# Kernel optimization log

Measured on AMD Instinct MI355X. Metric: run time of the kernel, lower is better.

The kernel has to match this reference:

```python
import jax, jax.numpy as jnp
import numpy as np

B, T, L, INPUT_DIM = 16, 128, 100, 100
EMB = 100
FEAT = INPUT_DIM + 3 * EMB          # 400
HID, OUT = 128, 50
RNN_IN = 2 * INPUT_DIM + 3 * L      # 500
VOCAB = 10000 + 2


def setup_inputs() -> dict:
    key = jax.random.key(0)
    ks = jax.random.split(key, 12)
    first = jax.random.normal(ks[0], (B, T, INPUT_DIM), jnp.float32)
    idx = jax.random.randint(ks[1], (B, T, 3 * L), 0, VOCAB).astype(jnp.float32)
    x = jnp.concatenate([first, idx], axis=2)  # [B,T,400]
    s = 0.05
    return {
        "x": x,
        "embed_nodes": jax.random.normal(ks[2], (VOCAB, EMB), jnp.float32) * s,
        "embed_paths": jax.random.normal(ks[3], (VOCAB, EMB), jnp.float32) * s,
        "W_t": jax.random.normal(ks[4], (FEAT, FEAT), jnp.float32) / np.sqrt(FEAT),
        "b_t": jnp.zeros((FEAT,), jnp.float32),
        "W_a": jax.random.normal(ks[5], (FEAT, 1), jnp.float32) / np.sqrt(FEAT),
        "b_a": jnp.zeros((1,), jnp.float32),
        "W_ih": jax.random.normal(ks[6], (4 * HID, RNN_IN), jnp.float32) / np.sqrt(RNN_IN),
        "W_hh": jax.random.normal(ks[7], (4 * HID, HID), jnp.float32) / np.sqrt(HID),
        "b_ih": jnp.zeros((4 * HID,), jnp.float32),
        "b_hh": jnp.zeros((4 * HID,), jnp.float32),
        "W_fc": jax.random.normal(ks[8], (HID, OUT), jnp.float32) / np.sqrt(HID),
        "b_fc": jnp.zeros((OUT,), jnp.float32),
    }


def _lstm(xs, W_ih, W_hh, b_ih, b_hh):
    # xs: [B,T,D] -> out [B,T,H]; PyTorch gate order i,f,g,o
    def step(carry, xt):
        h, c = carry
        g = xt @ W_ih.T + h @ W_hh.T + (b_ih + b_hh)  # [B,4H]
        i, f, gg, o = jnp.split(g, 4, axis=-1)
        c = jax.nn.sigmoid(f) * c + jax.nn.sigmoid(i) * jnp.tanh(gg)
        h = jax.nn.sigmoid(o) * jnp.tanh(c)
        return (h, c), h
    h0 = jnp.zeros((xs.shape[0], HID), xs.dtype)
    (_, _), hs = jax.lax.scan(step, (h0, h0), jnp.swapaxes(xs, 0, 1))
    return jnp.swapaxes(hs, 0, 1)


def reference(x, embed_nodes, embed_paths, W_t, b_t, W_a, b_a,
              W_ih, W_hh, b_ih, b_hh, W_fc, b_fc):
    first = x[:, :, :INPUT_DIM]                                   # [B,T,100]
    c2v = x[:, :, INPUT_DIM:INPUT_DIM + 3 * L].reshape(B, T, L, 3).astype(jnp.int32)
    s_emb = embed_nodes[c2v[..., 0]]                              # [B,T,L,100]
    e_emb = embed_nodes[c2v[..., 2]]
    p_emb = embed_paths[c2v[..., 1]]
    att_part = jnp.broadcast_to(first[:, :, None, :], (B, T, L, INPUT_DIM))
    full = jnp.concatenate([s_emb, e_emb, p_emb, att_part], axis=3)  # [B,T,L,400]
    # dropout skipped (deterministic reference == evaluating=True path)
    transformed = jnp.tanh(full @ W_t + b_t)
    ctx = transformed @ W_a + b_a                                 # [B,T,L,1]
    # faithful to nn.Softmax(dim=1): softmax over the sequence axis T
    attn = jax.nn.softmax(ctx, axis=1)
    code_vectors = jnp.sum(full * attn, axis=2)                   # [B,T,400]
    rnn_input = jnp.concatenate([first, code_vectors], axis=2)    # [B,T,500]
    out = _lstm(rnn_input, W_ih, W_hh, b_ih, b_hh)                # [B,T,128]
    return jax.nn.sigmoid(out @ W_fc + b_fc)                      # [B,T,50]
```

## Files before the change

### kernel.cpp

```cpp
#include <hip/hip_runtime.h>
#include <hip/hip_bf16.h>
#include <stdint.h>

#define B_     16
#define T_     128
#define L_     100
#define IN_    100
#define EMB_   100
#define FEAT_  400
#define HID_   128
#define OUT_   50
#define RNNIN_ 500
#define VOCAB_ 10002
#define BT_    2048
#define TBLK   157

#define S_T    (0.16f / 127.0f)
#define INVS_T (127.0f / 0.16f)
#define S_E    (0.30f / 127.0f)
#define INVS_E (127.0f / 0.30f)

typedef __attribute__((ext_vector_type(8))) short short8;
typedef __attribute__((ext_vector_type(4))) float f32x4;

__device__ __forceinline__ float fast_tanh(float x) {
    x = fminf(15.f, fmaxf(-15.f, x));
    float e = __expf(2.f * x);
    return (e - 1.f) * __builtin_amdgcn_rcpf(e + 1.f);
}
__device__ __forceinline__ float sigm(float x) {
    x = fminf(30.f, fmaxf(-30.f, x));
    float e = __expf(-x);
    return __builtin_amdgcn_rcpf(1.f + e);
}
__device__ __forceinline__ signed char q8(float v, float invs) {
    float t = fminf(127.f, fmaxf(-127.f, v * invs));
    return (signed char)__float2int_rn(t);
}
__device__ __forceinline__ int sb(unsigned int u, int k) {
    return (int)(signed char)(u >> (8 * k));
}

__global__ __launch_bounds__(256) void casts_k(
    const float* __restrict__ EN, const float* __restrict__ EP,
    const float* __restrict__ Wt, const float* __restrict__ Wih,
    const float* __restrict__ Whh,
    signed char* __restrict__ EN8, signed char* __restrict__ EP8,
    __hip_bfloat16* __restrict__ WtT, __hip_bfloat16* __restrict__ Wih_bf,
    __hip_bfloat16* __restrict__ Whh_bf)
{
    int t0 = blockIdx.x * 256 + threadIdx.x;
    const int stride = 1024 * 256;
    int n1 = VOCAB_ * 100;
    for (int i = t0; i < n1; i += stride) EN8[i] = q8(EN[i], INVS_E);
    for (int i = t0; i < n1; i += stride) EP8[i] = q8(EP[i], INVS_E);
    for (int i = t0; i < 4 * 400 * 128; i += stride) {
        int w = i / (400 * 128), rem = i - w * 400 * 128;
        int n = rem >> 7, k = rem & 127;
        WtT[i] = __float2bfloat16((k < 100) ? Wt[(size_t)(w * 100 + k) * 400 + n] : 0.f);
    }
    for (int i = t0; i < 512 * 512; i += stride) {
        int g = i >> 9, k = i & 511;
        Wih_bf[i] = __float2bfloat16((k < 500) ? Wih[(size_t)g * 500 + k] : 0.f);
    }
    for (int i = t0; i < 512 * 128; i += stride) Whh_bf[i] = __float2bfloat16(Whh[i]);
}

__device__ __forceinline__ void load_a100_f32(const float* __restrict__ arow,
                                              int kg, short8 af[4])
{
#pragma unroll
    for (int s = 0; s < 3; s++) {
        const float* p = arow + s * 32 + kg * 8;
#pragma unroll
        for (int j = 0; j < 8; j++)
            af[s][j] = (short)__bfloat16_as_ushort(__float2bfloat16(p[j]));
    }
    short8 z = {};
    af[3] = z;
    if (kg == 0) {
#pragma unroll
        for (int j = 0; j < 4; j++)
            af[3][j] = (short)__bfloat16_as_ushort(__float2bfloat16(arow[96 + j]));
    }
}

__global__ __launch_bounds__(256) void mm_k(
    const float* __restrict__ EN, const float* __restrict__ EP,
    const float* __restrict__ x, const __hip_bfloat16* __restrict__ WtT,
    const float* __restrict__ btb,
    signed char* __restrict__ Es, signed char* __restrict__ Ee,
    signed char* __restrict__ Ep, float* __restrict__ q)
{
    int blk = blockIdx.x, tid = threadIdx.x;
    int wave = tid >> 6, lane = tid & 63;
    int cl = lane & 15, kg = lane >> 4;

    if (blk < 3 * TBLK) {
        int which = blk / TBLK, mb = blk - which * TBLK;
        const float* A = (which == 2) ? EP : EN;
        signed char* outp = (which == 0) ? Es : ((which == 1) ? Ee : Ep);
        int r0 = mb * 64 + wave * 16;
        int ra = r0 + cl; if (ra > VOCAB_ - 1) ra = VOCAB_ - 1;
        short8 af[4];
        load_a100_f32(A + (size_t)ra * 100, kg, af);
        const __hip_bfloat16* Bp = WtT + (size_t)which * 400 * 128;
        for (int n0 = 0; n0 < 25; n0++) {
            const __hip_bfloat16* brow = Bp + (size_t)(n0 * 16 + cl) * 128 + kg * 8;
            f32x4 acc = (f32x4){0.f, 0.f, 0.f, 0.f};
            acc = __builtin_amdgcn_mfma_f32_16x16x32_bf16(af[0], *(const short8*)(brow), acc, 0, 0, 0);
            acc = __builtin_amdgcn_mfma_f32_16x16x32_bf16(af[1], *(const short8*)(brow + 32), acc, 0, 0, 0);
            acc = __builtin_amdgcn_mfma_f32_16x16x32_bf16(af[2], *(const short8*)(brow + 64), acc, 0, 0, 0);
            acc = __builtin_amdgcn_mfma_f32_16x16x32_bf16(af[3], *(const short8*)(brow + 96), acc, 0, 0, 0);
            int colj = n0 * 16 + cl;
#pragma unroll
            for (int r = 0; r < 4; r++) {
                int gr = r0 + kg * 4 + r;
                if (gr < VOCAB_)
                    outp[(size_t)gr * 400 + colj] = q8(acc[r], INVS_T);
            }
        }
    } else {
        int mb = blk - 3 * TBLK;
        int r0 = mb * 64 + wave * 16;
        short8 af[4];
        load_a100_f32(x + (size_t)(r0 + cl) * 400, kg, af);
        const __hip_bfloat16* Bp = WtT + (size_t)3 * 400 * 128;
        for (int n0 = 0; n0 < 25; n0++) {
            const __hip_bfloat16* brow = Bp + (size_t)(n0 * 16 + cl) * 128 + kg * 8;
            f32x4 acc = (f32x4){0.f, 0.f, 0.f, 0.f};
            acc = __builtin_amdgcn_mfma_f32_16x16x32_bf16(af[0], *(const short8*)(brow), acc, 0, 0, 0);
            acc = __builtin_amdgcn_mfma_f32_16x16x32_bf16(af[1], *(const short8*)(brow + 32), acc, 0, 0, 0);
            acc = __builtin_amdgcn_mfma_f32_16x16x32_bf16(af[2], *(const short8*)(brow + 64), acc, 0, 0, 0);
            acc = __builtin_amdgcn_mfma_f32_16x16x32_bf16(af[3], *(const short8*)(brow + 96), acc, 0, 0, 0);
            int colj = n0 * 16 + cl;
            float bb = btb[colj];
#pragma unroll
            for (int r = 0; r < 4; r++) {
                int gr = r0 + kg * 4 + r;
                q[(size_t)gr * 400 + colj] = acc[r] + bb;
            }
        }
    }
}

__global__ __launch_bounds__(256) void stage_a(
    const float* __restrict__ x,
    const signed char* __restrict__ Es8, const signed char* __restrict__ Ee8,
    const signed char* __restrict__ Ep8,
    const float* __restrict__ q, const float* __restrict__ Wa,
    float* __restrict__ ctx)
{
    __shared__ int idx_s[300];
    int bt = blockIdx.x, tid = threadIdx.x;
    const float* xr = x + (size_t)bt * 400 + 100;
    for (int i = tid; i < 300; i += 256) idx_s[i] = (int)xr[i];
    int lane = tid & 63, wave = tid >> 6;
    bool act = lane < 50;
    int j0 = lane * 8;
    float qv[8], wv[8];
    if (act) {
        float4 qa = *(const float4*)(q + (size_t)bt * 400 + j0);
        float4 qb = *(const float4*)(q + (size_t)bt * 400 + j0 + 4);
        float4 wa = *(const float4*)(Wa + j0);
        float4 wb = *(const float4*)(Wa + j0 + 4);
        qv[0]=qa.x; qv[1]=qa.y; qv[2]=qa.z; qv[3]=qa.w;
        qv[4]=qb.x; qv[5]=qb.y; qv[6]=qb.z; qv[7]=qb.w;
        wv[0]=wa.x; wv[1]=wa.y; wv[2]=wa.z; wv[3]=wa.w;
        wv[4]=wb.x; wv[5]=wb.y; wv[6]=wb.z; wv[7]=wb.w;
    } else {
#pragma unroll
        for (int jj = 0; jj < 8; jj++) { qv[jj] = 0.f; wv[jj] = 0.f; }
    }
    __syncthreads();
    for (int l = wave; l < 100; l += 4) {
        int i0 = idx_s[3 * l], i1 = idx_s[3 * l + 1], i2 = idx_s[3 * l + 2];
        float sum = 0.f;
        if (act) {
            uint2 a  = ((const uint2*)(Es8 + (size_t)i0 * 400))[lane];
            uint2 b  = ((const uint2*)(Ee8 + (size_t)i2 * 400))[lane];
            uint2 cc = ((const uint2*)(Ep8 + (size_t)i1 * 400))[lane];
            int zi[8];
#pragma unroll
            for (int k = 0; k < 4; k++) {
                zi[k]     = sb(a.x, k) + sb(b.x, k) + sb(cc.x, k);
                zi[4 + k] = sb(a.y, k) + sb(b.y, k) + sb(cc.y, k);
            }
#pragma unroll
            for (int jj = 0; jj < 8; jj++) {
                float z = fmaf((float)zi[jj], S_T, qv[jj]);
                sum = fmaf(fast_tanh(z), wv[jj], sum);
            }
        }
#pragma unroll
        for (int off = 32; off; off >>= 1) sum += __shfl_xor(sum, off);
        if (lane == 0) ctx[(size_t)bt * 100 + l] = sum;
    }
}

__global__ __launch_bounds__(256) void softmax_w(
    const float* __restrict__ ctx, float* __restrict__ attn)
{
    int wid = blockIdx.x * 4 + (threadIdx.x >> 6);
    int lane = threadIdx.x & 63;
    int b = wid / 100, l = wid - b * 100;
    size_t base = (size_t)b * 128 * 100 + l;
    float v0 = ctx[base + (size_t)lane * 100];
    float v1 = ctx[base + (size_t)(lane + 64) * 100];
    float m = fmaxf(v0, v1);
#pragma unroll
    for (int off = 32; off; off >>= 1) m = fmaxf(m, __shfl_xor(m, off));
    float e0 = __expf(v0 - m), e1 = __expf(v1 - m);
    float s = e0 + e1;
#pragma unroll
    for (int off = 32; off; off >>= 1) s += __shfl_xor(s, off);
    float rs = 1.f / s;
    attn[base + (size_t)lane * 100] = e0 * rs;
    attn[base + (size_t)(lane + 64) * 100] = e1 * rs;
}

__global__ __launch_bounds__(128) void stage_c(
    const float* __restrict__ x, const float* __restrict__ attn,
    const signed char* __restrict__ EN8, const signed char* __restrict__ EP8,
    __hip_bfloat16* __restrict__ rnn_bf)
{
    __shared__ float at[100];
    __shared__ int idx[300];
    int bt = blockIdx.x, tid = threadIdx.x;
    if (tid < 100) at[tid] = attn[(size_t)bt * 100 + tid];
    const float* xr = x + (size_t)bt * 400 + 100;
    for (int i = tid; i < 300; i += 128) idx[i] = (int)xr[i];
    __syncthreads();
    int d = tid;
    __hip_bfloat16* o = rnn_bf + (size_t)bt * 512;
    if (d < 100) {
        float as = 0.f, ae = 0.f, ap = 0.f, sa = 0.f;
#pragma unroll 4
        for (int l = 0; l < 100; l++) {
            float a = at[l]; sa += a;
            as = fmaf(a, (float)EN8[(size_t)idx[3 * l] * 100 + d], as);
            ae = fmaf(a, (float)EN8[(size_t)idx[3 * l + 2] * 100 + d], ae);
            ap = fmaf(a, (float)EP8[(size_t)idx[3 * l + 1] * 100 + d], ap);
        }
        float fi = x[(size_t)bt * 400 + d];
        o[d]       = __float2bfloat16(fi);
        o[100 + d] = __float2bfloat16(as * S_E);
        o[200 + d] = __float2bfloat16(ae * S_E);
        o[300 + d] = __float2bfloat16(ap * S_E);
        o[400 + d] = __float2bfloat16(fi * sa);
    } else if (d < 112) {
        o[400 + d] = __float2bfloat16(0.f);
    }
}

__global__ __launch_bounds__(512, 1) void lstm_k(
    const __hip_bfloat16* __restrict__ rnn_bf, const __hip_bfloat16* __restrict__ Wih_bf,
    const float* __restrict__ bih, const float* __restrict__ bhh,
    const __hip_bfloat16* __restrict__ Whh_bf,
    float* __restrict__ X, float* __restrict__ hs)
{
    int b = blockIdx.x, tid = threadIdx.x;
    int wave = tid >> 6, lane = tid & 63;
    int col = lane & 15, kg = lane >> 4;

    {
        int r0 = b * 128 + wave * 16;
        short8 af[16];
        const __hip_bfloat16* arow = rnn_bf + (size_t)(r0 + col) * 512 + kg * 8;
#pragma unroll
        for (int ks = 0; ks < 16; ks++) af[ks] = *(const short8*)(arow + ks * 32);
        for (int n0 = 0; n0 < 32; n0 += 2) {
            const __hip_bfloat16* b0 = Wih_bf + (size_t)(n0 * 16 + col) * 512 + kg * 8;
            const __hip_bfloat16* b1 = b0 + 16 * 512;
            f32x4 acA = (f32x4){0.f, 0.f, 0.f, 0.f};
            f32x4 acB = (f32x4){0.f, 0.f, 0.f, 0.f};
#pragma unroll
            for (int ks = 0; ks < 16; ks++) {
                acA = __builtin_amdgcn_mfma_f32_16x16x32_bf16(af[ks], *(const short8*)(b0 + ks * 32), acA, 0, 0, 0);
                acB = __builtin_amdgcn_mfma_f32_16x16x32_bf16(af[ks], *(const short8*)(b1 + ks * 32), acB, 0, 0, 0);
            }
            int c0 = n0 * 16 + col, c1 = c0 + 16;
            float bi0 = bih[c0] + bhh[c0];
            float bi1 = bih[c1] + bhh[c1];
#pragma unroll
            for (int r = 0; r < 4; r++) {
                int m = r0 + kg * 4 + r;
                X[(size_t)m * 512 + c0] = acA[r] + bi0;
                X[(size_t)m * 512 + c1] = acB[r] + bi1;
            }
        }
    }

    short8 bf[4][4];
#pragma unroll
    for (int n = 0; n < 4; n++) {
        int g = n * 128 + wave * 16 + col;
#pragma unroll
        for (int kk = 0; kk < 4; kk++)
            bf[n][kk] = *(const short8*)(Whh_bf + (size_t)g * 128 + kk * 32 + kg * 8);
    }

    __shared__ __hip_bfloat16 hbuf[2][128];
    __shared__ float Xs[16][512];
    __shared__ float hsb_s[16][128];
    float c = 0.f;
    if (tid < 128) hbuf[0][tid] = __float2bfloat16(0.f);
    const float* xb = X + (size_t)b * 128 * 512;
    float* hb = hs + (size_t)b * 128 * 128;
    int j = wave * 16 + col;
    int p = 0;

    __syncthreads();

    for (int tc = 0; tc < 8; tc++) {
        {
            const float* src = xb + (size_t)tc * 16 * 512 + tid;
#pragma unroll
            for (int k = 0; k < 16; k++) Xs[k][tid] = src[k * 512];
        }
        __syncthreads();

#pragma unroll 1
        for (int ts = 0; ts < 16; ts++) {
            short8 af[4];
            short8 zz = {};
#pragma unroll
            for (int kk = 0; kk < 4; kk++) {
                af[kk] = zz;
                if (col == 0) af[kk] = *(const short8*)(&hbuf[p][0] + kk * 32 + kg * 8);
            }
            f32x4 acc[4];
#pragma unroll
            for (int n = 0; n < 4; n++) acc[n] = (f32x4){0.f, 0.f, 0.f, 0.f};
#pragma unroll
            for (int kk = 0; kk < 4; kk++)
#pragma unroll
                for (int n = 0; n < 4; n++)
                    acc[n] = __builtin_amdgcn_mfma_f32_16x16x32_bf16(af[kk], bf[n][kk], acc[n], 0, 0, 0);

            if (lane < 16) {
                float pi = acc[0][0] + Xs[ts][j];
                float pf = acc[1][0] + Xs[ts][128 + j];
                float pg = acc[2][0] + Xs[ts][256 + j];
                float po = acc[3][0] + Xs[ts][384 + j];
                c = sigm(pf) * c + sigm(pi) * fast_tanh(pg);
                float hn = sigm(po) * fast_tanh(c);
                hbuf[p ^ 1][j] = __float2bfloat16(hn);
                hsb_s[ts][j] = hn;
            }
            __syncthreads();
            p ^= 1;
        }

        {
            float* dst = hb + (size_t)tc * 16 * 128;
#pragma unroll
            for (int k = 0; k < 4; k++) {
                int i = k * 512 + tid;
                dst[i] = hsb_s[i >> 7][i & 127];
            }
        }
    }
}

__global__ __launch_bounds__(64) void fc_k(
    const float* __restrict__ hs, const float* __restrict__ Wfc,
    const float* __restrict__ bfc, float* __restrict__ out)
{
    int r0 = blockIdx.x * 4, o = threadIdx.x;
    if (o >= 50) return;
    float acc[4] = {0.f, 0.f, 0.f, 0.f};
    for (int j = 0; j < 128; j++) {
        float wv = Wfc[j * 50 + o];
#pragma unroll
        for (int r = 0; r < 4; r++)
            acc[r] = fmaf(hs[(size_t)(r0 + r) * 128 + j], wv, acc[r]);
    }
    float bb = bfc[o];
#pragma unroll
    for (int r = 0; r < 4; r++) out[(size_t)(r0 + r) * 50 + o] = sigm(acc[r] + bb);
}

extern "C" void kernel_launch(void* const* d_in, const int* in_sizes, int n_in,
                              void* d_out, int out_size, void* d_ws, size_t ws_size,
                              hipStream_t stream) {
    const float* x   = (const float*)d_in[0];
    const float* EN  = (const float*)d_in[1];
    const float* EP  = (const float*)d_in[2];
    const float* Wt  = (const float*)d_in[3];
    const float* bt  = (const float*)d_in[4];
    const float* Wa  = (const float*)d_in[5];
    const float* Wih = (const float*)d_in[7];
    const float* Whh = (const float*)d_in[8];
    const float* bih = (const float*)d_in[9];
    const float* bhh = (const float*)d_in[10];
    const float* Wfc = (const float*)d_in[11];
    const float* bfc = (const float*)d_in[12];
    float* out = (float*)d_out;

    char* ws = (char*)d_ws;
    size_t off = 0;
    auto alloc = [&](size_t bytes) -> char* {
        char* p = ws + off;
        off = (off + bytes + 255) & ~(size_t)255;
        return p;
    };
    signed char* Es  = (signed char*)alloc((size_t)VOCAB_ * 400);
    signed char* Ee  = (signed char*)alloc((size_t)VOCAB_ * 400);
    signed char* Epb = (signed char*)alloc((size_t)VOCAB_ * 400);
    signed char* EN8 = (signed char*)alloc((size_t)VOCAB_ * 100);
    signed char* EP8 = (signed char*)alloc((size_t)VOCAB_ * 100);
    __hip_bfloat16* WtT    = (__hip_bfloat16*)alloc((size_t)4 * 400 * 128 * 2);
    __hip_bfloat16* Wih_bf = (__hip_bfloat16*)alloc((size_t)512 * 512 * 2);
    __hip_bfloat16* Whh_bf = (__hip_bfloat16*)alloc((size_t)512 * 128 * 2);
    __hip_bfloat16* rnn_bf = (__hip_bfloat16*)alloc((size_t)BT_ * 512 * 2);
    float* q    = (float*)alloc((size_t)BT_ * 400 * 4);
    float* ctx  = (float*)alloc((size_t)BT_ * 100 * 4);
    float* attn = (float*)alloc((size_t)BT_ * 100 * 4);
    float* X    = (float*)alloc((size_t)BT_ * 512 * 4);
    float* hsb  = (float*)alloc((size_t)BT_ * 128 * 4);

    casts_k<<<1024, 256, 0, stream>>>(EN, EP, Wt, Wih, Whh,
                                      EN8, EP8, WtT, Wih_bf, Whh_bf);
    mm_k<<<3 * TBLK + 32, 256, 0, stream>>>(EN, EP, x, WtT, bt,
                                            Es, Ee, Epb, q);
    stage_a<<<BT_, 256, 0, stream>>>(x, Es, Ee, Epb, q, Wa, ctx);
    softmax_w<<<400, 256, 0, stream>>>(ctx, attn);
    stage_c<<<BT_, 128, 0, stream>>>(x, attn, EN8, EP8, rnn_bf);
    lstm_k<<<B_, 512, 0, stream>>>(rnn_bf, Wih_bf, bih, bhh, Whh_bf, X, hsb);
    fc_k<<<BT_ / 4, 64, 0, stream>>>(hsb, Wfc, bfc, out);
}
```

Before: 314.3 us.

## Split LSTM input projection into separate GEMM kernel and drop int8 embedding casts

Moves the input-to-gate GEMM out of the 16-block LSTM kernel into its own 32-block kernel, so the projection runs across more compute units instead of only the 16 recurrence blocks. It also removes the int8 quantization pass over both embedding tables; stage_c now gathers fp32 embeddings directly, and the casts kernel shrinks to 256 blocks. The trade-off is an extra launch and fp32 gather traffic four times larger in stage_c, in exchange for skipping a full-table conversion every call and gaining precision.

```diff
diff --git a/kernel.cpp b/kernel.cpp
--- a/kernel.cpp
+++ b/kernel.cpp
@@ -17,8 +17,6 @@
 
 #define S_T    (0.16f / 127.0f)
 #define INVS_T (127.0f / 0.16f)
-#define S_E    (0.30f / 127.0f)
-#define INVS_E (127.0f / 0.30f)
 
 typedef __attribute__((ext_vector_type(8))) short short8;
 typedef __attribute__((ext_vector_type(4))) float f32x4;
@@ -42,18 +40,13 @@
 }
 
 __global__ __launch_bounds__(256) void casts_k(
-    const float* __restrict__ EN, const float* __restrict__ EP,
     const float* __restrict__ Wt, const float* __restrict__ Wih,
     const float* __restrict__ Whh,
-    signed char* __restrict__ EN8, signed char* __restrict__ EP8,
     __hip_bfloat16* __restrict__ WtT, __hip_bfloat16* __restrict__ Wih_bf,
     __hip_bfloat16* __restrict__ Whh_bf)
 {
     int t0 = blockIdx.x * 256 + threadIdx.x;
-    const int stride = 1024 * 256;
-    int n1 = VOCAB_ * 100;
-    for (int i = t0; i < n1; i += stride) EN8[i] = q8(EN[i], INVS_E);
-    for (int i = t0; i < n1; i += stride) EP8[i] = q8(EP[i], INVS_E);
+    const int stride = 256 * 256;
     for (int i = t0; i < 4 * 400 * 128; i += stride) {
         int w = i / (400 * 128), rem = i - w * 400 * 128;
         int n = rem >> 7, k = rem & 127;
@@ -221,7 +214,7 @@
 
 __global__ __launch_bounds__(128) void stage_c(
     const float* __restrict__ x, const float* __restrict__ attn,
-    const signed char* __restrict__ EN8, const signed char* __restrict__ EP8,
+    const float* __restrict__ EN, const float* __restrict__ EP,
     __hip_bfloat16* __restrict__ rnn_bf)
 {
     __shared__ float at[100];
@@ -238,58 +231,65 @@
 #pragma unroll 4
         for (int l = 0; l < 100; l++) {
             float a = at[l]; sa += a;
-            as = fmaf(a, (float)EN8[(size_t)idx[3 * l] * 100 + d], as);
-            ae = fmaf(a, (float)EN8[(size_t)idx[3 * l + 2] * 100 + d], ae);
-            ap = fmaf(a, (float)EP8[(size_t)idx[3 * l + 1] * 100 + d], ap);
+            as = fmaf(a, EN[(size_t)idx[3 * l] * 100 + d], as);
+            ae = fmaf(a, EN[(size_t)idx[3 * l + 2] * 100 + d], ae);
+            ap = fmaf(a, EP[(size_t)idx[3 * l + 1] * 100 + d], ap);
         }
         float fi = x[(size_t)bt * 400 + d];
         o[d]       = __float2bfloat16(fi);
-        o[100 + d] = __float2bfloat16(as * S_E);
-        o[200 + d] = __float2bfloat16(ae * S_E);
-        o[300 + d] = __float2bfloat16(ap * S_E);
+        o[100 + d] = __float2bfloat16(as);
+        o[200 + d] = __float2bfloat16(ae);
+        o[300 + d] = __float2bfloat16(ap);
         o[400 + d] = __float2bfloat16(fi * sa);
     } else if (d < 112) {
         o[400 + d] = __float2bfloat16(0.f);
     }
 }
 
-__global__ __launch_bounds__(512, 1) void lstm_k(
+__global__ __launch_bounds__(256) void gemm_x(
     const __hip_bfloat16* __restrict__ rnn_bf, const __hip_bfloat16* __restrict__ Wih_bf,
     const float* __restrict__ bih, const float* __restrict__ bhh,
-    const __hip_bfloat16* __restrict__ Whh_bf,
-    float* __restrict__ X, float* __restrict__ hs)
+    float* __restrict__ X)
+{
+    int blk = blockIdx.x, tid = threadIdx.x;
+    int wave = tid >> 6, lane = tid & 63;
+    int cl = lane & 15, kg = lane >> 4;
+    int r0 = blk * 64 + wave * 16;
+
+    short8 af[16];
+    const __hip_bfloat16* arow = rnn_bf + (size_t)(r0 + cl) * 512 + kg * 8;
+#pragma unroll
+    for (int ks = 0; ks < 16; ks++) af[ks] = *(const short8*)(arow + ks * 32);
+
+    for (int n0 = 0; n0 < 32; n0 += 2) {
+        const __hip_bfloat16* b0 = Wih_bf + (size_t)(n0 * 16 + cl) * 512 + kg * 8;
+        const __hip_bfloat16* b1 = b0 + 16 * 512;
+        f32x4 acA = (f32x4){0.f, 0.f, 0.f, 0.f};
+        f32x4 acB = (f32x4){0.f, 0.f, 0.f, 0.f};
+#pragma unroll
+        for (int ks = 0; ks < 16; ks++) {
+            acA = __builtin_amdgcn_mfma_f32_16x16x32_bf16(af[ks], *(const short8*)(b0 + ks * 32), acA, 0, 0, 0);
+            acB = __builtin_amdgcn_mfma_f32_16x16x32_bf16(af[ks], *(const short8*)(b1 + ks * 32), acB, 0, 0, 0);
+        }
+        int c0 = n0 * 16 + cl, c1 = c0 + 16;
+        float bi0 = bih[c0] + bhh[c0];
+        float bi1 = bih[c1] + bhh[c1];
+#pragma unroll
+        for (int r = 0; r < 4; r++) {
+            int m = r0 + kg * 4 + r;
+            X[(size_t)m * 512 + c0] = acA[r] + bi0;
+            X[(size_t)m * 512 + c1] = acB[r] + bi1;
+        }
+    }
+}
+
+__global__ __launch_bounds__(512, 1) void lstm_k(
+    const float* __restrict__ X, const __hip_bfloat16* __restrict__ Whh_bf,
+    float* __restrict__ hs)
 {
     int b = blockIdx.x, tid = threadIdx.x;
     int wave = tid >> 6, lane = tid & 63;
     int col = lane & 15, kg = lane >> 4;
-
-    {
-        int r0 = b * 128 + wave * 16;
-        short8 af[16];
-        const __hip_bfloat16* arow = rnn_bf + (size_t)(r0 + col) * 512 + kg * 8;
-#pragma unroll
-        for (int ks = 0; ks < 16; ks++) af[ks] = *(const short8*)(arow + ks * 32);
-        for (int n0 = 0; n0 < 32; n0 += 2) {
-            const __hip_bfloat16* b0 = Wih_bf + (size_t)(n0 * 16 + col) * 512 + kg * 8;
-            const __hip_bfloat16* b1 = b0 + 16 * 512;
-            f32x4 acA = (f32x4){0.f, 0.f, 0.f, 0.f};
-            f32x4 acB = (f32x4){0.f, 0.f, 0.f, 0.f};
-#pragma unroll
-            for (int ks = 0; ks < 16; ks++) {
-                acA = __builtin_amdgcn_mfma_f32_16x16x32_bf16(af[ks], *(const short8*)(b0 + ks * 32), acA, 0, 0, 0);
-                acB = __builtin_amdgcn_mfma_f32_16x16x32_bf16(af[ks], *(const short8*)(b1 + ks * 32), acB, 0, 0, 0);
-            }
-            int c0 = n0 * 16 + col, c1 = c0 + 16;
-            float bi0 = bih[c0] + bhh[c0];
-            float bi1 = bih[c1] + bhh[c1];
-#pragma unroll
-            for (int r = 0; r < 4; r++) {
-                int m = r0 + kg * 4 + r;
-                X[(size_t)m * 512 + c0] = acA[r] + bi0;
-                X[(size_t)m * 512 + c1] = acB[r] + bi1;
-            }
-        }
-    }
 
     short8 bf[4][4];
 #pragma unroll
@@ -408,8 +408,6 @@
     signed char* Es  = (signed char*)alloc((size_t)VOCAB_ * 400);
     signed char* Ee  = (signed char*)alloc((size_t)VOCAB_ * 400);
     signed char* Epb = (signed char*)alloc((size_t)VOCAB_ * 400);
-    signed char* EN8 = (signed char*)alloc((size_t)VOCAB_ * 100);
-    signed char* EP8 = (signed char*)alloc((size_t)VOCAB_ * 100);
     __hip_bfloat16* WtT    = (__hip_bfloat16*)alloc((size_t)4 * 400 * 128 * 2);
     __hip_bfloat16* Wih_bf = (__hip_bfloat16*)alloc((size_t)512 * 512 * 2);
     __hip_bfloat16* Whh_bf = (__hip_bfloat16*)alloc((size_t)512 * 128 * 2);
@@ -420,13 +418,13 @@
     float* X    = (float*)alloc((size_t)BT_ * 512 * 4);
     float* hsb  = (float*)alloc((size_t)BT_ * 128 * 4);
 
-    casts_k<<<1024, 256, 0, stream>>>(EN, EP, Wt, Wih, Whh,
-                                      EN8, EP8, WtT, Wih_bf, Whh_bf);
+    casts_k<<<256, 256, 0, stream>>>(Wt, Wih, Whh, WtT, Wih_bf, Whh_bf);
     mm_k<<<3 * TBLK + 32, 256, 0, stream>>>(EN, EP, x, WtT, bt,
                                             Es, Ee, Epb, q);
     stage_a<<<BT_, 256, 0, stream>>>(x, Es, Ee, Epb, q, Wa, ctx);
     softmax_w<<<400, 256, 0, stream>>>(ctx, attn);
-    stage_c<<<BT_, 128, 0, stream>>>(x, attn, EN8, EP8, rnn_bf);
-    lstm_k<<<B_, 512, 0, stream>>>(rnn_bf, Wih_bf, bih, bhh, Whh_bf, X, hsb);
+    stage_c<<<BT_, 128, 0, stream>>>(x, attn, EN, EP, rnn_bf);
+    gemm_x<<<32, 256, 0, stream>>>(rnn_bf, Wih_bf, bih, bhh, X);
+    lstm_k<<<B_, 512, 0, stream>>>(X, Whh_bf, hsb);
     fc_k<<<BT_ / 4, 64, 0, stream>>>(hsb, Wfc, bfc, out);
 }
```

New measurement: 275.0 us. 1.14x faster.
